# Kernel tuning notes

Measured on AMD Instinct MI355X. Metric: run time of the kernel, lower is better.

Reference implementation:

```python
import jax, jax.numpy as jnp
import numpy as np
import math

B, L, D, P = 2, 2048, 256, 32

def _lin_init(key, fan_in, shape):
    return jax.random.normal(key, shape, dtype=jnp.float32) / np.float32(math.sqrt(fan_in))

def setup_inputs() -> dict:
    key = jax.random.key(0)
    ks = jax.random.split(key, 16)
    return {
        "x": jax.random.normal(ks[0], (B, L, D), dtype=jnp.float32),
        "pos_phases": jax.random.normal(ks[1], (L, P), dtype=jnp.float32) * np.float32(math.pi),
        "w_pos_value": _lin_init(ks[2], D, (D, D)), "b_pos_value": jnp.zeros((D,), jnp.float32),
        "w_key": _lin_init(ks[3], D, (D, P)), "b_key": jnp.zeros((P,), jnp.float32),
        "w_kv": _lin_init(ks[4], D, (D, D)), "b_kv": jnp.zeros((D,), jnp.float32),
        "w_vg1": _lin_init(ks[5], 2 * D, (2 * D, D)), "b_vg1": jnp.zeros((D,), jnp.float32),
        "w_vg2": _lin_init(ks[6], D, (D, 1)), "b_vg2": jnp.zeros((1,), jnp.float32),
        "w_bg1": _lin_init(ks[7], D, (D, D // 2)), "b_bg1": jnp.zeros((D // 2,), jnp.float32),
        "w_bg2": _lin_init(ks[8], D // 2, (D // 2, 2)), "b_bg2": jnp.zeros((2,), jnp.float32),
        "ln_r_g": jnp.ones((D,), jnp.float32), "ln_r_b": jnp.zeros((D,), jnp.float32),
        "w_r1": _lin_init(ks[9], D, (D, 2 * D)), "b_r1": jnp.zeros((2 * D,), jnp.float32),
        "w_r2": _lin_init(ks[10], 2 * D, (2 * D, D)), "b_r2": jnp.zeros((D,), jnp.float32),
        "ln_o_g": jnp.ones((D,), jnp.float32), "ln_o_b": jnp.zeros((D,), jnp.float32),
        "w_out": _lin_init(ks[11], D, (D, D)), "b_out": jnp.zeros((D,), jnp.float32),
    }

def _ln(z, g, b, eps=1e-5):
    mu = z.mean(-1, keepdims=True)
    var = ((z - mu) ** 2).mean(-1, keepdims=True)
    return (z - mu) * jax.lax.rsqrt(var + eps) * g + b

def _shift1(z):
    # torch.roll(shifts=1, dims=1) then zero first position == shift right with zero pad
    return jnp.concatenate([jnp.zeros_like(z[:, :1]), z[:, :-1]], axis=1)

def reference(x, pos_phases, w_pos_value, b_pos_value, w_key, b_key, w_kv, b_kv,
              w_vg1, b_vg1, w_vg2, b_vg2, w_bg1, b_bg1, w_bg2, b_bg2,
              ln_r_g, ln_r_b, w_r1, b_r1, w_r2, b_r2, ln_o_g, ln_o_b, w_out, b_out):
    Bv, Lv, Dv = x.shape
    Pv = pos_phases.shape[1]
    inv_sqrt_p = np.float32(1.0 / math.sqrt(Pv))

    # --- positional memory ---
    pos_phasors = jnp.exp(1j * pos_phases)                      # (L,P) complex64
    pos_values = (x @ w_pos_value + b_pos_value).astype(jnp.complex64)  # (B,L,D)
    pos_bound = pos_phasors[None, :, :, None] * pos_values[:, :, None, :]  # (B,L,P,D)
    pos_memory = jnp.cumsum(pos_bound, axis=1)
    pos_query = jnp.exp(-1j * pos_phases)                       # (L,P)
    pos_retrieved = (pos_memory * pos_query[None, :, :, None]).sum(axis=2).real * inv_sqrt_p

    # --- content-based KV memory ---
    key_phases = jnp.tanh(x @ w_key + b_key) * np.float32(math.pi)  # (B,L,P)
    key_phasors = jnp.exp(1j * key_phases)
    kv_values = (x @ w_kv + b_kv).astype(jnp.complex64)         # (B,L,D)

    x_shifted = _shift1(x)
    gate_input = jnp.concatenate([x, x_shifted], axis=-1)       # (B,L,2D)
    h = jax.nn.gelu(gate_input @ w_vg1 + b_vg1, approximate=False)
    value_gates = jax.nn.sigmoid(h @ w_vg2 + b_vg2)             # (B,L,1)

    key_phasors_shifted = _shift1(key_phasors)                  # (B,L,P)
    kv_bound = (key_phasors_shifted[..., None] * kv_values[:, :, None, :]) \
               * value_gates[:, :, :, None].astype(jnp.complex64)  # (B,L,P,D)
    kv_memory = jnp.cumsum(kv_bound, axis=1)
    gate_cumsum = jnp.maximum(jnp.cumsum(value_gates, axis=1), 1.0)  # (B,L,1)
    kv_query = jnp.exp(-1j * key_phases)                        # (B,L,P)
    kv_retrieved = (kv_memory * kv_query[..., None]).sum(axis=2).real
    kv_retrieved = kv_retrieved / (jnp.sqrt(gate_cumsum) * np.float32(math.sqrt(Pv)))

    # --- blend, refine, output ---
    bg_h = jax.nn.gelu(x @ w_bg1 + b_bg1, approximate=False)
    blend = jax.nn.softmax(bg_h @ w_bg2 + b_bg2, axis=-1)       # (B,L,2)
    blended = blend[..., 0:1] * pos_retrieved + blend[..., 1:2] * kv_retrieved

    refined = jax.nn.gelu(_ln(blended, ln_r_g, ln_r_b) @ w_r1 + b_r1, approximate=False) @ w_r2 + b_r2
    return x + (_ln(refined, ln_o_g, ln_o_b) @ w_out + b_out)
```

## Files before the change

### kernel.cpp

```cpp
#include <hip/hip_runtime.h>
#include <math.h>

#define B_ 2
#define L_ 2048
#define D_ 256
#define P_ 32
#define NC_ 64
#define CL_ 32

#define INV_SQRT_P 0.17677669529663687f
#define PI_F 3.14159265358979323846f

typedef __attribute__((ext_vector_type(8))) short bf16x8;
typedef __attribute__((ext_vector_type(4))) float f32x4;

__device__ __forceinline__ float gelu_exact(float x){
    return 0.5f * x * (1.0f + erff(x * 0.70710678118654752f));
}

__device__ __forceinline__ unsigned short f2bf(float f){
    unsigned int u = __float_as_uint(f);
    u += 0x7FFFu + ((u >> 16) & 1u);
    return (unsigned short)(u >> 16);
}

__global__ __launch_bounds__(256) void k_prep(
    const float* __restrict__ pos_phases,
    const float* __restrict__ w_pv, const float* __restrict__ w_kv,
    const float* __restrict__ w_vg1, const float* __restrict__ w_bg1,
    const float* __restrict__ w_r1, const float* __restrict__ w_r2,
    const float* __restrict__ w_out, const float* __restrict__ w_key,
    unsigned short* __restrict__ wq,
    float* __restrict__ cpos, float* __restrict__ spos)
{
    int id = blockIdx.x * 256 + threadIdx.x;
    if (id < 630784){
        const float* src; int N; int local;
        if (id < 65536)       { src = w_pv;  N = 256; local = id; }
        else if (id < 131072) { src = w_kv;  N = 256; local = id - 65536; }
        else if (id < 262144) { src = w_vg1; N = 256; local = id - 131072; }
        else if (id < 294912) { src = w_bg1; N = 128; local = id - 262144; }
        else if (id < 425984) { src = w_r1;  N = 512; local = id - 294912; }
        else if (id < 557056) { src = w_r2;  N = 256; local = id - 425984; }
        else if (id < 622592) { src = w_out; N = 256; local = id - 557056; }
        else                  { src = w_key; N = 32;  local = id - 622592; }
        int j = local & 7, lane = (local >> 3) & 63, tile = local >> 9;
        int NT = N >> 4;
        int nt = tile % NT, kt = tile / NT;
        int row = kt * 32 + ((lane >> 4) << 3) + j;
        int col = nt * 16 + (lane & 15);
        wq[id] = f2bf(src[(size_t)row * N + col]);
    } else {
        int idx = id - 630784;
        float s, c;
        sincosf(pos_phases[idx], &s, &c);
        cpos[idx] = c;
        spos[idx] = s;
    }
}

__global__ __launch_bounds__(512) void k_proj(
    const float* __restrict__ x,
    const unsigned short* __restrict__ wq,
    const float* __restrict__ b_pv, const float* __restrict__ b_kv,
    const float* __restrict__ b_vg1,
    const float* __restrict__ w_vg2, const float* __restrict__ b_vg2,
    const float* __restrict__ b_bg1,
    const float* __restrict__ w_bg2, const float* __restrict__ b_bg2,
    const float* __restrict__ b_key,
    float* __restrict__ pv, float* __restrict__ kvv,
    float* __restrict__ ck, float* __restrict__ sk,
    float* __restrict__ vg, float* __restrict__ blend0, float* __restrict__ blend1)
{
    __shared__ float hbuf[16][257];
    __shared__ float bhbuf[16][129];
    __shared__ float kph[16][33];
    __shared__ float red[16][17], red2[16][17], red3[16][17];

    const int i = threadIdx.x;
    const int lane = i & 63, w = i >> 6;
    const int b = blockIdx.x >> 7, lt = blockIdx.x & 127, l0 = lt * 16;
    const int g = lane >> 4, c = lane & 15;

    bf16x8 xa[8], xs[8];
    {
        int row  = l0 + (lane & 15);
        int rowp = row - 1;
        const float* xr = x + (size_t)(b * L_ + row) * D_ + ((lane >> 4) << 3);
        #pragma unroll
        for (int kt = 0; kt < 8; ++kt){
            float4 a0 = *(const float4*)(xr + kt * 32);
            float4 a1 = *(const float4*)(xr + kt * 32 + 4);
            bf16x8 v;
            v[0] = (short)f2bf(a0.x); v[1] = (short)f2bf(a0.y);
            v[2] = (short)f2bf(a0.z); v[3] = (short)f2bf(a0.w);
            v[4] = (short)f2bf(a1.x); v[5] = (short)f2bf(a1.y);
            v[6] = (short)f2bf(a1.z); v[7] = (short)f2bf(a1.w);
            xa[kt] = v;
        }
        if (rowp >= 0){
            const float* xp = x + (size_t)(b * L_ + rowp) * D_ + ((lane >> 4) << 3);
            #pragma unroll
            for (int kt = 0; kt < 8; ++kt){
                float4 a0 = *(const float4*)(xp + kt * 32);
                float4 a1 = *(const float4*)(xp + kt * 32 + 4);
                bf16x8 v;
                v[0] = (short)f2bf(a0.x); v[1] = (short)f2bf(a0.y);
                v[2] = (short)f2bf(a0.z); v[3] = (short)f2bf(a0.w);
                v[4] = (short)f2bf(a1.x); v[5] = (short)f2bf(a1.y);
                v[6] = (short)f2bf(a1.z); v[7] = (short)f2bf(a1.w);
                xs[kt] = v;
            }
        } else {
            #pragma unroll
            for (int kt = 0; kt < 8; ++kt){
                bf16x8 v;
                #pragma unroll
                for (int j = 0; j < 8; ++j) v[j] = 0;
                xs[kt] = v;
            }
        }
    }

    const unsigned short* wpv  = wq;
    const unsigned short* wkv  = wq + 65536;
    const unsigned short* wvg1 = wq + 131072;
    const unsigned short* wbg1 = wq + 262144;
    const unsigned short* wkey = wq + 622592;

    for (int jb = w; jb < 58; jb += 8){
        f32x4 acc = {0.f, 0.f, 0.f, 0.f};
        if (jb < 2){
            int nt = jb;
            #pragma unroll
            for (int kt = 0; kt < 8; ++kt){
                bf16x8 bf = *(const bf16x8*)(wkey + (kt * 2 + nt) * 512 + lane * 8);
                acc = __builtin_amdgcn_mfma_f32_16x16x32_bf16(xa[kt], bf, acc, 0, 0, 0);
            }
            float bb = b_key[nt * 16 + c];
            #pragma unroll
            for (int r = 0; r < 4; ++r)
                kph[4 * g + r][nt * 16 + c] = acc[r] + bb;
        } else if (jb < 18){
            int nt = jb - 2;
            #pragma unroll
            for (int kt = 0; kt < 8; ++kt){
                bf16x8 bf = *(const bf16x8*)(wpv + (kt * 16 + nt) * 512 + lane * 8);
                acc = __builtin_amdgcn_mfma_f32_16x16x32_bf16(xa[kt], bf, acc, 0, 0, 0);
            }
            float bb = b_pv[nt * 16 + c];
            #pragma unroll
            for (int r = 0; r < 4; ++r)
                pv[(size_t)(b * L_ + l0 + 4 * g + r) * D_ + nt * 16 + c] = acc[r] + bb;
        } else if (jb < 34){
            int nt = jb - 18;
            #pragma unroll
            for (int kt = 0; kt < 8; ++kt){
                bf16x8 bf = *(const bf16x8*)(wkv + (kt * 16 + nt) * 512 + lane * 8);
                acc = __builtin_amdgcn_mfma_f32_16x16x32_bf16(xa[kt], bf, acc, 0, 0, 0);
            }
            float bb = b_kv[nt * 16 + c];
            #pragma unroll
            for (int r = 0; r < 4; ++r)
                kvv[(size_t)(b * L_ + l0 + 4 * g + r) * D_ + nt * 16 + c] = acc[r] + bb;
        } else if (jb < 50){
            int nt = jb - 34;
            #pragma unroll
            for (int kt = 0; kt < 8; ++kt){
                bf16x8 bf = *(const bf16x8*)(wvg1 + (kt * 16 + nt) * 512 + lane * 8);
                acc = __builtin_amdgcn_mfma_f32_16x16x32_bf16(xa[kt], bf, acc, 0, 0, 0);
            }
            #pragma unroll
            for (int kt = 8; kt < 16; ++kt){
                bf16x8 bf = *(const bf16x8*)(wvg1 + (kt * 16 + nt) * 512 + lane * 8);
                acc = __builtin_amdgcn_mfma_f32_16x16x32_bf16(xs[kt - 8], bf, acc, 0, 0, 0);
            }
            float bb = b_vg1[nt * 16 + c];
            #pragma unroll
            for (int r = 0; r < 4; ++r)
                hbuf[4 * g + r][nt * 16 + c] = gelu_exact(acc[r] + bb);
        } else {
            int nt = jb - 50;
            #pragma unroll
            for (int kt = 0; kt < 8; ++kt){
                bf16x8 bf = *(const bf16x8*)(wbg1 + (kt * 8 + nt) * 512 + lane * 8);
                acc = __builtin_amdgcn_mfma_f32_16x16x32_bf16(xa[kt], bf, acc, 0, 0, 0);
            }
            float bb = b_bg1[nt * 16 + c];
            #pragma unroll
            for (int r = 0; r < 4; ++r)
                bhbuf[4 * g + r][nt * 16 + c] = gelu_exact(acc[r] + bb);
        }
    }
    __syncthreads();

    {
        int t = i >> 5, p = i & 31;
        float a = tanhf(kph[t][p]) * PI_F;
        float s, cc;
        sincosf(a, &s, &cc);
        ck[(size_t)(b * L_ + l0 + t) * P_ + p] = cc;
        sk[(size_t)(b * L_ + l0 + t) * P_ + p] = s;
    }

    if (i < 256){
        int t = i >> 4, c2 = i & 15;
        float s = 0.f;
        #pragma unroll
        for (int m = 0; m < 16; ++m){ int dd = c2 + 16 * m; s += hbuf[t][dd] * w_vg2[dd]; }
        red[t][c2] = s;
    } else {
        int ii = i - 256;
        int t = ii >> 4, c2 = ii & 15;
        float s0 = 0.f, s1 = 0.f;
        #pragma unroll
        for (int m = 0; m < 8; ++m){
            int jj = c2 + 16 * m;
            float v = bhbuf[t][jj];
            s0 += v * w_bg2[jj * 2 + 0];
            s1 += v * w_bg2[jj * 2 + 1];
        }
        red2[t][c2] = s0; red3[t][c2] = s1;
    }
    __syncthreads();
    if (i < 16){
        float s = 0.f;
        #pragma unroll
        for (int c2 = 0; c2 < 16; ++c2) s += red[i][c2];
        s += b_vg2[0];
        vg[b * L_ + l0 + i] = 1.0f / (1.0f + expf(-s));
    } else if (i < 32){
        int t = i - 16;
        float s0 = 0.f, s1 = 0.f;
        #pragma unroll
        for (int c2 = 0; c2 < 16; ++c2){ s0 += red2[t][c2]; s1 += red3[t][c2]; }
        s0 += b_bg2[0]; s1 += b_bg2[1];
        float mx = fmaxf(s0, s1);
        float e0 = expf(s0 - mx), e1 = expf(s1 - mx);
        float inv = 1.0f / (e0 + e1);
        blend0[b * L_ + l0 + t] = e0 * inv;
        blend1[b * L_ + l0 + t] = e1 * inv;
    }
}

__global__ __launch_bounds__(256) void k_scan1(
    const float* __restrict__ cpos, const float* __restrict__ spos,
    const float* __restrict__ ck, const float* __restrict__ sk,
    const float* __restrict__ pv, const float* __restrict__ kvv,
    const float* __restrict__ vg,
    float* __restrict__ posSr, float* __restrict__ posSi,
    float* __restrict__ kvSr, float* __restrict__ kvSi,
    float* __restrict__ rnorm)
{
    const int z = blockIdx.z;
    const int c = blockIdx.x, b = blockIdx.y;
    const int i = threadIdx.x;
    if (z == 8){
        if (c != 0) return;
        float loc[8];
        float run = 0.f;
        #pragma unroll
        for (int m = 0; m < 8; ++m){ run += vg[b * L_ + i * 8 + m]; loc[m] = run; }
        __shared__ float part[256];
        part[i] = run;
        __syncthreads();
        for (int off = 1; off < 256; off <<= 1){
            float t = (i >= off) ? part[i - off] : 0.0f;
            __syncthreads();
            part[i] += t;
            __syncthreads();
        }
        float excl = part[i] - run;
        #pragma unroll
        for (int m = 0; m < 8; ++m){
            float gc = fmaxf(excl + loc[m], 1.0f);
            rnorm[b * L_ + i * 8 + m] = rsqrtf(gc) * INV_SQRT_P;
        }
        return;
    }
    const int type = z >> 2, pg = z & 3;
    const int d = i;
    const int p0 = pg * 8;
    float Sr[8], Si[8];
    #pragma unroll
    for (int j = 0; j < 8; ++j){ Sr[j] = 0.f; Si[j] = 0.f; }

    if (type == 0){
        for (int l = 0; l < CL_; ++l){
            int row = c * CL_ + l;
            float v = pv[(size_t)(b * L_ + row) * D_ + d];
            float4 c0 = *(const float4*)(cpos + row * P_ + p0);
            float4 c1 = *(const float4*)(cpos + row * P_ + p0 + 4);
            float4 s0 = *(const float4*)(spos + row * P_ + p0);
            float4 s1 = *(const float4*)(spos + row * P_ + p0 + 4);
            Sr[0] = fmaf(c0.x, v, Sr[0]); Si[0] = fmaf(s0.x, v, Si[0]);
            Sr[1] = fmaf(c0.y, v, Sr[1]); Si[1] = fmaf(s0.y, v, Si[1]);
            Sr[2] = fmaf(c0.z, v, Sr[2]); Si[2] = fmaf(s0.z, v, Si[2]);
            Sr[3] = fmaf(c0.w, v, Sr[3]); Si[3] = fmaf(s0.w, v, Si[3]);
            Sr[4] = fmaf(c1.x, v, Sr[4]); Si[4] = fmaf(s1.x, v, Si[4]);
            Sr[5] = fmaf(c1.y, v, Sr[5]); Si[5] = fmaf(s1.y, v, Si[5]);
            Sr[6] = fmaf(c1.z, v, Sr[6]); Si[6] = fmaf(s1.z, v, Si[6]);
            Sr[7] = fmaf(c1.w, v, Sr[7]); Si[7] = fmaf(s1.w, v, Si[7]);
        }
        #pragma unroll
        for (int j = 0; j < 8; ++j){
            size_t o = (size_t)((b * NC_ + c) * P_ + p0 + j) * D_ + d;
            posSr[o] = Sr[j]; posSi[o] = Si[j];
        }
    } else {
        float pc[8], ps[8];
        int srow = c * CL_ - 1;
        if (srow >= 0){
            float4 c0 = *(const float4*)(ck + ((size_t)b * L_ + srow) * P_ + p0);
            float4 c1 = *(const float4*)(ck + ((size_t)b * L_ + srow) * P_ + p0 + 4);
            float4 s0 = *(const float4*)(sk + ((size_t)b * L_ + srow) * P_ + p0);
            float4 s1 = *(const float4*)(sk + ((size_t)b * L_ + srow) * P_ + p0 + 4);
            pc[0]=c0.x; pc[1]=c0.y; pc[2]=c0.z; pc[3]=c0.w;
            pc[4]=c1.x; pc[5]=c1.y; pc[6]=c1.z; pc[7]=c1.w;
            ps[0]=s0.x; ps[1]=s0.y; ps[2]=s0.z; ps[3]=s0.w;
            ps[4]=s1.x; ps[5]=s1.y; ps[6]=s1.z; ps[7]=s1.w;
        } else {
            #pragma unroll
            for (int j = 0; j < 8; ++j){ pc[j] = 0.f; ps[j] = 0.f; }
        }
        for (int l = 0; l < CL_; ++l){
            int row = c * CL_ + l;
            float vv = kvv[(size_t)(b * L_ + row) * D_ + d] * vg[b * L_ + row];
            float4 c0 = *(const float4*)(ck + ((size_t)b * L_ + row) * P_ + p0);
            float4 c1 = *(const float4*)(ck + ((size_t)b * L_ + row) * P_ + p0 + 4);
            float4 s0 = *(const float4*)(sk + ((size_t)b * L_ + row) * P_ + p0);
            float4 s1 = *(const float4*)(sk + ((size_t)b * L_ + row) * P_ + p0 + 4);
            #pragma unroll
            for (int j = 0; j < 8; ++j){
                Sr[j] = fmaf(pc[j], vv, Sr[j]);
                Si[j] = fmaf(ps[j], vv, Si[j]);
            }
            pc[0]=c0.x; pc[1]=c0.y; pc[2]=c0.z; pc[3]=c0.w;
            pc[4]=c1.x; pc[5]=c1.y; pc[6]=c1.z; pc[7]=c1.w;
            ps[0]=s0.x; ps[1]=s0.y; ps[2]=s0.z; ps[3]=s0.w;
            ps[4]=s1.x; ps[5]=s1.y; ps[6]=s1.z; ps[7]=s1.w;
        }
        #pragma unroll
        for (int j = 0; j < 8; ++j){
            size_t o = (size_t)((b * NC_ + c) * P_ + p0 + j) * D_ + d;
            kvSr[o] = Sr[j]; kvSi[o] = Si[j];
        }
    }
}

__global__ __launch_bounds__(256) void k_prefix(
    float* __restrict__ posSr, float* __restrict__ posSi,
    float* __restrict__ kvSr, float* __restrict__ kvSi)
{
    __shared__ float4 tot_s[64][4];
    const int colLocal = threadIdx.x >> 2, seg = threadIdx.x & 3;
    const int col = blockIdx.x * 64 + colLocal;
    const int a = col >> 12;
    const int rem = col & 4095;
    const int b = rem >> 11;
    const int pd = (rem & 2047) * 4;
    float* A = (a == 0) ? posSr : (a == 1) ? posSi : (a == 2) ? kvSr : kvSi;
    float* base = A + (size_t)b * NC_ * (P_ * D_) + pd;

    float4 t[16];
    #pragma unroll
    for (int k = 0; k < 16; ++k)
        t[k] = *(const float4*)(base + (size_t)(seg * 16 + k) * (P_ * D_));
    float4 tot = {0.f, 0.f, 0.f, 0.f};
    #pragma unroll
    for (int k = 0; k < 16; ++k){
        tot.x += t[k].x; tot.y += t[k].y; tot.z += t[k].z; tot.w += t[k].w;
    }
    tot_s[colLocal][seg] = tot;
    __syncthreads();
    float4 run = {0.f, 0.f, 0.f, 0.f};
    #pragma unroll
    for (int s = 0; s < 3; ++s){
        if (s < seg){
            float4 v = tot_s[colLocal][s];
            run.x += v.x; run.y += v.y; run.z += v.z; run.w += v.w;
        }
    }
    #pragma unroll
    for (int k = 0; k < 16; ++k){
        float4 cur = t[k];
        *(float4*)(base + (size_t)(seg * 16 + k) * (P_ * D_)) = run;
        run.x += cur.x; run.y += cur.y; run.z += cur.z; run.w += cur.w;
    }
}

__global__ __launch_bounds__(256) void k_retrieve(
    const float* __restrict__ cpos, const float* __restrict__ spos,
    const float* __restrict__ ck, const float* __restrict__ sk,
    const float* __restrict__ pv, const float* __restrict__ kvv,
    const float* __restrict__ vg, const float* __restrict__ rnorm,
    const float* __restrict__ posSr, const float* __restrict__ posSi,
    const float* __restrict__ kvSr, const float* __restrict__ kvSi,
    float* __restrict__ posret, float* __restrict__ kvret)
{
    const int z = blockIdx.z;
    const int c = blockIdx.x, b = blockIdx.y;
    const int type = z >> 2, dquad = z & 3;
    const int lane = threadIdx.x & 63, wv = threadIdx.x >> 6;
    const int pg = lane >> 4, dl = lane & 15;
    const int d = dquad * 64 + wv * 16 + dl;
    const int p0 = pg * 8;

    float Sr[8], Si[8];

    if (type == 0){
        #pragma unroll
        for (int j = 0; j < 8; ++j){
            size_t o = (size_t)((b * NC_ + c) * P_ + p0 + j) * D_ + d;
            Sr[j] = posSr[o]; Si[j] = posSi[o];
        }
        for (int l = 0; l < CL_; ++l){
            int row = c * CL_ + l;
            float v = pv[(size_t)(b * L_ + row) * D_ + d];
            float4 c0 = *(const float4*)(cpos + row * P_ + p0);
            float4 c1 = *(const float4*)(cpos + row * P_ + p0 + 4);
            float4 s0 = *(const float4*)(spos + row * P_ + p0);
            float4 s1 = *(const float4*)(spos + row * P_ + p0 + 4);
            float r0 = 0.f, r1 = 0.f, r2 = 0.f, r3 = 0.f;
            Sr[0] = fmaf(c0.x, v, Sr[0]); r0 = fmaf(c0.x, Sr[0], r0);
            Si[0] = fmaf(s0.x, v, Si[0]); r1 = fmaf(s0.x, Si[0], r1);
            Sr[1] = fmaf(c0.y, v, Sr[1]); r2 = fmaf(c0.y, Sr[1], r2);
            Si[1] = fmaf(s0.y, v, Si[1]); r3 = fmaf(s0.y, Si[1], r3);
            Sr[2] = fmaf(c0.z, v, Sr[2]); r0 = fmaf(c0.z, Sr[2], r0);
            Si[2] = fmaf(s0.z, v, Si[2]); r1 = fmaf(s0.z, Si[2], r1);
            Sr[3] = fmaf(c0.w, v, Sr[3]); r2 = fmaf(c0.w, Sr[3], r2);
            Si[3] = fmaf(s0.w, v, Si[3]); r3 = fmaf(s0.w, Si[3], r3);
            Sr[4] = fmaf(c1.x, v, Sr[4]); r0 = fmaf(c1.x, Sr[4], r0);
            Si[4] = fmaf(s1.x, v, Si[4]); r1 = fmaf(s1.x, Si[4], r1);
            Sr[5] = fmaf(c1.y, v, Sr[5]); r2 = fmaf(c1.y, Sr[5], r2);
            Si[5] = fmaf(s1.y, v, Si[5]); r3 = fmaf(s1.y, Si[5], r3);
            Sr[6] = fmaf(c1.z, v, Sr[6]); r0 = fmaf(c1.z, Sr[6], r0);
            Si[6] = fmaf(s1.z, v, Si[6]); r1 = fmaf(s1.z, Si[6], r1);
            Sr[7] = fmaf(c1.w, v, Sr[7]); r2 = fmaf(c1.w, Sr[7], r2);
            Si[7] = fmaf(s1.w, v, Si[7]); r3 = fmaf(s1.w, Si[7], r3);
            float r = (r0 + r1) + (r2 + r3);
            r += __shfl_xor(r, 16, 64);
            r += __shfl_xor(r, 32, 64);
            if (pg == 0)
                posret[(size_t)(b * L_ + row) * D_ + d] = r * INV_SQRT_P;
        }
    } else {
        #pragma unroll
        for (int j = 0; j < 8; ++j){
            size_t o = (size_t)((b * NC_ + c) * P_ + p0 + j) * D_ + d;
            Sr[j] = kvSr[o]; Si[j] = kvSi[o];
        }
        float pc[8], ps[8];
        int srow = c * CL_ - 1;
        if (srow >= 0){
            float4 c0 = *(const float4*)(ck + ((size_t)b * L_ + srow) * P_ + p0);
            float4 c1 = *(const float4*)(ck + ((size_t)b * L_ + srow) * P_ + p0 + 4);
            float4 s0 = *(const float4*)(sk + ((size_t)b * L_ + srow) * P_ + p0);
            float4 s1 = *(const float4*)(sk + ((size_t)b * L_ + srow) * P_ + p0 + 4);
            pc[0]=c0.x; pc[1]=c0.y; pc[2]=c0.z; pc[3]=c0.w;
            pc[4]=c1.x; pc[5]=c1.y; pc[6]=c1.z; pc[7]=c1.w;
            ps[0]=s0.x; ps[1]=s0.y; ps[2]=s0.z; ps[3]=s0.w;
            ps[4]=s1.x; ps[5]=s1.y; ps[6]=s1.z; ps[7]=s1.w;
        } else {
            #pragma unroll
            for (int j = 0; j < 8; ++j){ pc[j] = 0.f; ps[j] = 0.f; }
        }
        for (int l = 0; l < CL_; ++l){
            int row = c * CL_ + l;
            float vv = kvv[(size_t)(b * L_ + row) * D_ + d] * vg[b * L_ + row];
            float rn = rnorm[b * L_ + row];
            float4 c0 = *(const float4*)(ck + ((size_t)b * L_ + row) * P_ + p0);
            float4 c1 = *(const float4*)(ck + ((size_t)b * L_ + row) * P_ + p0 + 4);
            float4 s0 = *(const float4*)(sk + ((size_t)b * L_ + row) * P_ + p0);
            float4 s1 = *(const float4*)(sk + ((size_t)b * L_ + row) * P_ + p0 + 4);
            float qc[8], qs[8];
            qc[0]=c0.x; qc[1]=c0.y; qc[2]=c0.z; qc[3]=c0.w;
            qc[4]=c1.x; qc[5]=c1.y; qc[6]=c1.z; qc[7]=c1.w;
            qs[0]=s0.x; qs[1]=s0.y; qs[2]=s0.z; qs[3]=s0.w;
            qs[4]=s1.x; qs[5]=s1.y; qs[6]=s1.z; qs[7]=s1.w;
            float r0 = 0.f, r1 = 0.f, r2 = 0.f, r3 = 0.f;
            #pragma unroll
            for (int j = 0; j < 8; ++j){
                Sr[j] = fmaf(pc[j], vv, Sr[j]);
                Si[j] = fmaf(ps[j], vv, Si[j]);
                if (j & 1){ r2 = fmaf(qc[j], Sr[j], r2); r3 = fmaf(qs[j], Si[j], r3); }
                else      { r0 = fmaf(qc[j], Sr[j], r0); r1 = fmaf(qs[j], Si[j], r1); }
                pc[j] = qc[j]; ps[j] = qs[j];
            }
            float r = (r0 + r1) + (r2 + r3);
            r += __shfl_xor(r, 16, 64);
            r += __shfl_xor(r, 32, 64);
            if (pg == 0)
                kvret[(size_t)(b * L_ + row) * D_ + d] = r * rn;
        }
    }
}

__global__ __launch_bounds__(512) void k_final(
    const float* __restrict__ x,
    const float* __restrict__ posret, const float* __restrict__ kvret,
    const float* __restrict__ blend0, const float* __restrict__ blend1,
    const unsigned short* __restrict__ wq,
    const float* __restrict__ ln_r_g, const float* __restrict__ ln_r_b,
    const float* __restrict__ b_r1, const float* __restrict__ b_r2,
    const float* __restrict__ ln_o_g, const float* __restrict__ ln_o_b,
    const float* __restrict__ b_out,
    float* __restrict__ out)
{
    __shared__ float zbuf[16][257];
    __shared__ __align__(16) unsigned short aA[8][512];
    __shared__ __align__(16) unsigned short aH[16][512];
    __shared__ float red[16][17], red2[16][17];
    __shared__ float mu[16], rs[16];

    const int i = threadIdx.x, lane = i & 63, w = i >> 6;
    const int b = blockIdx.x >> 7, l0 = (blockIdx.x & 127) * 16;
    const int g = lane >> 4, c = lane & 15;
    const unsigned short* wr1  = wq + 294912;
    const unsigned short* wr2  = wq + 425984;
    const unsigned short* wout = wq + 557056;

    {
        int t = i >> 5, c0 = (i & 31) * 8;
        size_t base = (size_t)(b * L_ + l0 + t) * D_ + c0;
        float w0 = blend0[b * L_ + l0 + t], w1 = blend1[b * L_ + l0 + t];
        #pragma unroll
        for (int m = 0; m < 8; ++m)
            zbuf[t][c0 + m] = w0 * posret[base + m] + w1 * kvret[base + m];
    }
    __syncthreads();

    if (i < 256){
        int t = i >> 4, c2 = i & 15;
        float s = 0.f, s2 = 0.f;
        #pragma unroll
        for (int m = 0; m < 16; ++m){ float v = zbuf[t][c2 + 16 * m]; s += v; s2 += v * v; }
        red[t][c2] = s; red2[t][c2] = s2;
    }
    __syncthreads();
    if (i < 16){
        float s = 0.f, s2 = 0.f;
        #pragma unroll
        for (int c2 = 0; c2 < 16; ++c2){ s += red[i][c2]; s2 += red2[i][c2]; }
        float mean = s * (1.0f / 256.0f);
        float var  = s2 * (1.0f / 256.0f) - mean * mean;
        mu[i] = mean; rs[i] = rsqrtf(var + 1e-5f);
    }
    __syncthreads();

    {
        int kt = i >> 6;
        int t2 = lane & 15, kb = kt * 32 + ((lane >> 4) << 3);
        float m_ = mu[t2], r_ = rs[t2];
        bf16x8 v8;
        #pragma unroll
        for (int j = 0; j < 8; ++j){
            int k = kb + j;
            float v = (zbuf[t2][k] - m_) * r_ * ln_r_g[k] + ln_r_b[k];
            v8[j] = (short)f2bf(v);
        }
        *(bf16x8*)&aA[kt][lane * 8] = v8;
    }
    __syncthreads();

    {
        bf16x8 afr[8];
        #pragma unroll
        for (int kt = 0; kt < 8; ++kt) afr[kt] = *(const bf16x8*)&aA[kt][lane * 8];
        for (int q = 0; q < 4; ++q){
            int nt = w + 8 * q;
            f32x4 acc = {0.f, 0.f, 0.f, 0.f};
            #pragma unroll
            for (int kt = 0; kt < 8; ++kt){
                bf16x8 bf = *(const bf16x8*)(wr1 + (kt * 32 + nt) * 512 + lane * 8);
                acc = __builtin_amdgcn_mfma_f32_16x16x32_bf16(afr[kt], bf, acc, 0, 0, 0);
            }
            float bb = b_r1[nt * 16 + c];
            #pragma unroll
            for (int r = 0; r < 4; ++r){
                float hv = gelu_exact(acc[r] + bb);
                int t = 4 * g + r, hcol = nt * 16 + c;
// ... 63 lines not shown
        #pragma unroll
        for (int kt = 0; kt < 8; ++kt) azr[kt] = *(const bf16x8*)&aA[kt][lane * 8];
        for (int q = 0; q < 2; ++q){
            int nt = w + 8 * q;
            f32x4 acc = {0.f, 0.f, 0.f, 0.f};
            #pragma unroll
            for (int kt = 0; kt < 8; ++kt){
                bf16x8 bf = *(const bf16x8*)(wout + (kt * 16 + nt) * 512 + lane * 8);
                acc = __builtin_amdgcn_mfma_f32_16x16x32_bf16(azr[kt], bf, acc, 0, 0, 0);
            }
            float bb = b_out[nt * 16 + c];
            #pragma unroll
            for (int r = 0; r < 4; ++r){
                size_t o = (size_t)(b * L_ + l0 + 4 * g + r) * D_ + nt * 16 + c;
                out[o] = x[o] + acc[r] + bb;
            }
        }
    }
}

extern "C" void kernel_launch(void* const* d_in, const int* in_sizes, int n_in,
                              void* d_out, int out_size, void* d_ws, size_t ws_size,
                              hipStream_t stream) {
    const float* x          = (const float*)d_in[0];
    const float* pos_phases = (const float*)d_in[1];
    const float* w_pv       = (const float*)d_in[2];
    const float* b_pv       = (const float*)d_in[3];
    const float* w_key      = (const float*)d_in[4];
    const float* b_key      = (const float*)d_in[5];
    const float* w_kv       = (const float*)d_in[6];
    const float* b_kv       = (const float*)d_in[7];
    const float* w_vg1      = (const float*)d_in[8];
    const float* b_vg1      = (const float*)d_in[9];
    const float* w_vg2      = (const float*)d_in[10];
    const float* b_vg2      = (const float*)d_in[11];
    const float* w_bg1      = (const float*)d_in[12];
    const float* b_bg1      = (const float*)d_in[13];
    const float* w_bg2      = (const float*)d_in[14];
    const float* b_bg2      = (const float*)d_in[15];
    const float* ln_r_g     = (const float*)d_in[16];
    const float* ln_r_b     = (const float*)d_in[17];
    const float* w_r1       = (const float*)d_in[18];
    const float* b_r1       = (const float*)d_in[19];
    const float* w_r2       = (const float*)d_in[20];
    const float* b_r2       = (const float*)d_in[21];
    const float* ln_o_g     = (const float*)d_in[22];
    const float* ln_o_b     = (const float*)d_in[23];
    const float* w_out      = (const float*)d_in[24];
    const float* b_out      = (const float*)d_in[25];
    float* out = (float*)d_out;

    float* ws = (float*)d_ws;
    size_t off = 0;
    float* cpos   = ws + off; off += (size_t)L_ * P_;
    float* spos   = ws + off; off += (size_t)L_ * P_;
    float* pv     = ws + off; off += (size_t)B_ * L_ * D_;
    float* kvv    = ws + off; off += (size_t)B_ * L_ * D_;
    float* ck     = ws + off; off += (size_t)B_ * L_ * P_;
    float* sk     = ws + off; off += (size_t)B_ * L_ * P_;
    float* vg     = ws + off; off += (size_t)B_ * L_;
    float* rnorm  = ws + off; off += (size_t)B_ * L_;
    float* blend0 = ws + off; off += (size_t)B_ * L_;
    float* blend1 = ws + off; off += (size_t)B_ * L_;
    float* posret = ws + off; off += (size_t)B_ * L_ * D_;
    float* kvret  = ws + off; off += (size_t)B_ * L_ * D_;
    float* posSr  = ws + off; off += (size_t)B_ * NC_ * P_ * D_;
    float* posSi  = ws + off; off += (size_t)B_ * NC_ * P_ * D_;
    float* kvSr   = ws + off; off += (size_t)B_ * NC_ * P_ * D_;
    float* kvSi   = ws + off; off += (size_t)B_ * NC_ * P_ * D_;
    unsigned short* wq = (unsigned short*)(ws + off); off += 630784 / 2;

    k_prep<<<2720, 256, 0, stream>>>(pos_phases,
        w_pv, w_kv, w_vg1, w_bg1, w_r1, w_r2, w_out, w_key,
        wq, cpos, spos);

    k_proj<<<B_ * 128, 512, 0, stream>>>(x, wq,
        b_pv, b_kv, b_vg1, w_vg2, b_vg2, b_bg1, w_bg2, b_bg2, b_key,
        pv, kvv, ck, sk, vg, blend0, blend1);

    k_scan1<<<dim3(NC_, B_, 9), 256, 0, stream>>>(cpos, spos, ck, sk, pv, kvv, vg,
                                                  posSr, posSi, kvSr, kvSi, rnorm);

    k_prefix<<<256, 256, 0, stream>>>(posSr, posSi, kvSr, kvSi);

    k_retrieve<<<dim3(NC_, B_, 8), 256, 0, stream>>>(cpos, spos, ck, sk, pv, kvv,
                                                     vg, rnorm,
                                                     posSr, posSi, kvSr, kvSi,
                                                     posret, kvret);

    k_final<<<B_ * 128, 512, 0, stream>>>(x, posret, kvret, blend0, blend1, wq,
        ln_r_g, ln_r_b, b_r1, b_r2, ln_o_g, ln_o_b, b_out, out);
}
```

Before: 89.07 us.

## Replace chunked complex scan with causal-masked MFMA attention formulation

Measured after the change: 148.5 us. +66.7%, slower.

```diff
diff --git a/kernel.cpp b/kernel.cpp
--- a/kernel.cpp
+++ b/kernel.cpp
@@ -5,14 +5,13 @@
 #define L_ 2048
 #define D_ 256
 #define P_ 32
-#define NC_ 64
-#define CL_ 32
 
 #define INV_SQRT_P 0.17677669529663687f
 #define PI_F 3.14159265358979323846f
 
 typedef __attribute__((ext_vector_type(8))) short bf16x8;
 typedef __attribute__((ext_vector_type(4))) float f32x4;
+typedef __attribute__((ext_vector_type(4))) unsigned short u16x4;
 
 __device__ __forceinline__ float gelu_exact(float x){
     return 0.5f * x * (1.0f + erff(x * 0.70710678118654752f));
@@ -31,7 +30,7 @@
     const float* __restrict__ w_r1, const float* __restrict__ w_r2,
     const float* __restrict__ w_out, const float* __restrict__ w_key,
     unsigned short* __restrict__ wq,
-    float* __restrict__ cpos, float* __restrict__ spos)
+    unsigned short* __restrict__ phib_pos)
 {
     int id = blockIdx.x * 256 + threadIdx.x;
     if (id < 630784){
@@ -52,10 +51,11 @@
         wq[id] = f2bf(src[(size_t)row * N + col]);
     } else {
         int idx = id - 630784;
+        int l = idx >> 5, p = idx & 31;
         float s, c;
         sincosf(pos_phases[idx], &s, &c);
-        cpos[idx] = c;
-        spos[idx] = s;
+        phib_pos[(size_t)l * 64 + p]      = f2bf(c);
+        phib_pos[(size_t)l * 64 + 32 + p] = f2bf(s);
     }
 }
 
@@ -68,14 +68,16 @@
     const float* __restrict__ b_bg1,
     const float* __restrict__ w_bg2, const float* __restrict__ b_bg2,
     const float* __restrict__ b_key,
-    float* __restrict__ pv, float* __restrict__ kvv,
-    float* __restrict__ ck, float* __restrict__ sk,
+    unsigned short* __restrict__ pvT, unsigned short* __restrict__ kvvT,
+    unsigned short* __restrict__ phib_kv,
     float* __restrict__ vg, float* __restrict__ blend0, float* __restrict__ blend1)
 {
     __shared__ float hbuf[16][257];
+    __shared__ float kvbuf[16][257];
     __shared__ float bhbuf[16][129];
     __shared__ float kph[16][33];
     __shared__ float red[16][17], red2[16][17], red3[16][17];
+    __shared__ float vgs[16];
 
     const int i = threadIdx.x;
     const int lane = i & 63, w = i >> 6;
@@ -149,9 +151,11 @@
                 acc = __builtin_amdgcn_mfma_f32_16x16x32_bf16(xa[kt], bf, acc, 0, 0, 0);
             }
             float bb = b_pv[nt * 16 + c];
-            #pragma unroll
-            for (int r = 0; r < 4; ++r)
-                pv[(size_t)(b * L_ + l0 + 4 * g + r) * D_ + nt * 16 + c] = acc[r] + bb;
+            int d = nt * 16 + c;
+            u16x4 pk;
+            pk[0] = f2bf(acc[0] + bb); pk[1] = f2bf(acc[1] + bb);
+            pk[2] = f2bf(acc[2] + bb); pk[3] = f2bf(acc[3] + bb);
+            *(u16x4*)(pvT + (size_t)(b * 256 + d) * 2048 + l0 + 4 * g) = pk;
         } else if (jb < 34){
             int nt = jb - 18;
             #pragma unroll
@@ -162,7 +166,7 @@
             float bb = b_kv[nt * 16 + c];
             #pragma unroll
             for (int r = 0; r < 4; ++r)
-                kvv[(size_t)(b * L_ + l0 + 4 * g + r) * D_ + nt * 16 + c] = acc[r] + bb;
+                kvbuf[4 * g + r][nt * 16 + c] = acc[r] + bb;
         } else if (jb < 50){
             int nt = jb - 34;
             #pragma unroll
@@ -199,8 +203,9 @@
         float a = tanhf(kph[t][p]) * PI_F;
         float s, cc;
         sincosf(a, &s, &cc);
-        ck[(size_t)(b * L_ + l0 + t) * P_ + p] = cc;
-        sk[(size_t)(b * L_ + l0 + t) * P_ + p] = s;
+        size_t rowo = (size_t)(b * L_ + l0 + t) * 64;
+        phib_kv[rowo + p]      = f2bf(cc);
+        phib_kv[rowo + 32 + p] = f2bf(s);
     }
 
     if (i < 256){
@@ -228,7 +233,9 @@
         #pragma unroll
         for (int c2 = 0; c2 < 16; ++c2) s += red[i][c2];
         s += b_vg2[0];
-        vg[b * L_ + l0 + i] = 1.0f / (1.0f + expf(-s));
+        float gv = 1.0f / (1.0f + expf(-s));
+        vg[b * L_ + l0 + i] = gv;
+        vgs[i] = gv;
     } else if (i < 32){
         int t = i - 16;
         float s0 = 0.f, s1 = 0.f;
@@ -241,265 +248,171 @@
         blend0[b * L_ + l0 + t] = e0 * inv;
         blend1[b * L_ + l0 + t] = e1 * inv;
     }
-}
-
-__global__ __launch_bounds__(256) void k_scan1(
-    const float* __restrict__ cpos, const float* __restrict__ spos,
-    const float* __restrict__ ck, const float* __restrict__ sk,
-    const float* __restrict__ pv, const float* __restrict__ kvv,
-    const float* __restrict__ vg,
-    float* __restrict__ posSr, float* __restrict__ posSi,
-    float* __restrict__ kvSr, float* __restrict__ kvSi,
-    float* __restrict__ rnorm)
+    __syncthreads();
+
+    {
+        int d = i & 255, tg = i >> 8;
+        bf16x8 pk;
+        #pragma unroll
+        for (int m = 0; m < 8; ++m){
+            int tok = tg * 8 + m;
+            pk[m] = (short)f2bf(kvbuf[tok][d] * vgs[tok]);
+        }
+        *(bf16x8*)(kvvT + (size_t)(b * 256 + d) * 2048 + l0 + tg * 8) = pk;
+    }
+}
+
+__global__ __launch_bounds__(256) void k_gatecum(const float* __restrict__ vg,
+                                                 float* __restrict__ rnorm){
+    int b = blockIdx.x, i = threadIdx.x;
+    float loc[8];
+    float run = 0.f;
+    #pragma unroll
+    for (int m = 0; m < 8; ++m){ run += vg[b * L_ + i * 8 + m]; loc[m] = run; }
+    __shared__ float part[256];
+    part[i] = run;
+    __syncthreads();
+    for (int off = 1; off < 256; off <<= 1){
+        float t = (i >= off) ? part[i - off] : 0.0f;
+        __syncthreads();
+        part[i] += t;
+        __syncthreads();
+    }
+    float excl = part[i] - run;
+    #pragma unroll
+    for (int m = 0; m < 8; ++m){
+        float gc = fmaxf(excl + loc[m], 1.0f);
+        rnorm[b * L_ + i * 8 + m] = rsqrtf(gc) * INV_SQRT_P;
+    }
+}
+
+__global__ __launch_bounds__(256) void k_flash(
+    const unsigned short* __restrict__ phib_pos,
+    const unsigned short* __restrict__ phib_kv,
+    const unsigned short* __restrict__ pvT,
+    const unsigned short* __restrict__ kvvT,
+    const float* __restrict__ rnorm,
+    const float* __restrict__ blend0, const float* __restrict__ blend1,
+    float* __restrict__ blended)
 {
-    const int z = blockIdx.z;
-    const int c = blockIdx.x, b = blockIdx.y;
-    const int i = threadIdx.x;
-    if (z == 8){
-        if (c != 0) return;
-        float loc[8];
-        float run = 0.f;
-        #pragma unroll
-        for (int m = 0; m < 8; ++m){ run += vg[b * L_ + i * 8 + m]; loc[m] = run; }
-        __shared__ float part[256];
-        part[i] = run;
-        __syncthreads();
-        for (int off = 1; off < 256; off <<= 1){
-            float t = (i >= off) ? part[i - off] : 0.0f;
-            __syncthreads();
-            part[i] += t;
-            __syncthreads();
-        }
-        float excl = part[i] - run;
-        #pragma unroll
-        for (int m = 0; m < 8; ++m){
-            float gc = fmaxf(excl + loc[m], 1.0f);
-            rnorm[b * L_ + i * 8 + m] = rsqrtf(gc) * INV_SQRT_P;
-        }
-        return;
-    }
-    const int type = z >> 2, pg = z & 3;
-    const int d = i;
-    const int p0 = pg * 8;
-    float Sr[8], Si[8];
+    __shared__ float redb[4][16][132];
+    __shared__ __align__(16) unsigned short scrP[4][16][40];
+    __shared__ __align__(16) unsigned short scrK[4][16][40];
+
+    const int qt = 127 - (blockIdx.x & 127);
+    const int dhalf = blockIdx.x >> 7;
+    const int b = blockIdx.y;
+    const int w = threadIdx.x >> 6, lane = threadIdx.x & 63;
+    const int g = lane >> 4, c = lane & 15;
+    const int q0 = qt * 16, d0 = dhalf * 128;
+
+    bf16x8 aqp[2], aqk[2];
+    {
+        const unsigned short* pp = phib_pos + (size_t)(q0 + c) * 64 + 8 * g;
+        aqp[0] = *(const bf16x8*)(pp);
+        aqp[1] = *(const bf16x8*)(pp + 32);
+        const unsigned short* pk = phib_kv + (size_t)(b * L_ + q0 + c) * 64 + 8 * g;
+        aqk[0] = *(const bf16x8*)(pk);
+        aqk[1] = *(const bf16x8*)(pk + 32);
+    }
+    f32x4 accP[8], accK[8];
     #pragma unroll
-    for (int j = 0; j < 8; ++j){ Sr[j] = 0.f; Si[j] = 0.f; }
-
-    if (type == 0){
-        for (int l = 0; l < CL_; ++l){
-            int row = c * CL_ + l;
-            float v = pv[(size_t)(b * L_ + row) * D_ + d];
-            float4 c0 = *(const float4*)(cpos + row * P_ + p0);
-            float4 c1 = *(const float4*)(cpos + row * P_ + p0 + 4);
-            float4 s0 = *(const float4*)(spos + row * P_ + p0);
-            float4 s1 = *(const float4*)(spos + row * P_ + p0 + 4);
-            Sr[0] = fmaf(c0.x, v, Sr[0]); Si[0] = fmaf(s0.x, v, Si[0]);
-            Sr[1] = fmaf(c0.y, v, Sr[1]); Si[1] = fmaf(s0.y, v, Si[1]);
-            Sr[2] = fmaf(c0.z, v, Sr[2]); Si[2] = fmaf(s0.z, v, Si[2]);
-            Sr[3] = fmaf(c0.w, v, Sr[3]); Si[3] = fmaf(s0.w, v, Si[3]);
-            Sr[4] = fmaf(c1.x, v, Sr[4]); Si[4] = fmaf(s1.x, v, Si[4]);
-            Sr[5] = fmaf(c1.y, v, Sr[5]); Si[5] = fmaf(s1.y, v, Si[5]);
-            Sr[6] = fmaf(c1.z, v, Sr[6]); Si[6] = fmaf(s1.z, v, Si[6]);
-            Sr[7] = fmaf(c1.w, v, Sr[7]); Si[7] = fmaf(s1.w, v, Si[7]);
-        }
-        #pragma unroll
-        for (int j = 0; j < 8; ++j){
-            size_t o = (size_t)((b * NC_ + c) * P_ + p0 + j) * D_ + d;
-            posSr[o] = Sr[j]; posSi[o] = Si[j];
-        }
-    } else {
-        float pc[8], ps[8];
-        int srow = c * CL_ - 1;
-        if (srow >= 0){
-            float4 c0 = *(const float4*)(ck + ((size_t)b * L_ + srow) * P_ + p0);
-            float4 c1 = *(const float4*)(ck + ((size_t)b * L_ + srow) * P_ + p0 + 4);
-            float4 s0 = *(const float4*)(sk + ((size_t)b * L_ + srow) * P_ + p0);
-            float4 s1 = *(const float4*)(sk + ((size_t)b * L_ + srow) * P_ + p0 + 4);
-            pc[0]=c0.x; pc[1]=c0.y; pc[2]=c0.z; pc[3]=c0.w;
-            pc[4]=c1.x; pc[5]=c1.y; pc[6]=c1.z; pc[7]=c1.w;
-            ps[0]=s0.x; ps[1]=s0.y; ps[2]=s0.z; ps[3]=s0.w;
-            ps[4]=s1.x; ps[5]=s1.y; ps[6]=s1.z; ps[7]=s1.w;
-        } else {
-            #pragma unroll
-            for (int j = 0; j < 8; ++j){ pc[j] = 0.f; ps[j] = 0.f; }
-        }
-        for (int l = 0; l < CL_; ++l){
-            int row = c * CL_ + l;
-            float vv = kvv[(size_t)(b * L_ + row) * D_ + d] * vg[b * L_ + row];
-            float4 c0 = *(const float4*)(ck + ((size_t)b * L_ + row) * P_ + p0);
-            float4 c1 = *(const float4*)(ck + ((size_t)b * L_ + row) * P_ + p0 + 4);
-            float4 s0 = *(const float4*)(sk + ((size_t)b * L_ + row) * P_ + p0);
-            float4 s1 = *(const float4*)(sk + ((size_t)b * L_ + row) * P_ + p0 + 4);
-            #pragma unroll
-            for (int j = 0; j < 8; ++j){
-                Sr[j] = fmaf(pc[j], vv, Sr[j]);
-                Si[j] = fmaf(ps[j], vv, Si[j]);
-            }
-            pc[0]=c0.x; pc[1]=c0.y; pc[2]=c0.z; pc[3]=c0.w;
-            pc[4]=c1.x; pc[5]=c1.y; pc[6]=c1.z; pc[7]=c1.w;
-            ps[0]=s0.x; ps[1]=s0.y; ps[2]=s0.z; ps[3]=s0.w;
-            ps[4]=s1.x; ps[5]=s1.y; ps[6]=s1.z; ps[7]=s1.w;
-        }
-        #pragma unroll
-        for (int j = 0; j < 8; ++j){
-            size_t o = (size_t)((b * NC_ + c) * P_ + p0 + j) * D_ + d;
-            kvSr[o] = Sr[j]; kvSi[o] = Si[j];
-        }
-    }
-}
-
-__global__ __launch_bounds__(256) void k_prefix(
-    float* __restrict__ posSr, float* __restrict__ posSi,
-    float* __restrict__ kvSr, float* __restrict__ kvSi)
-{
-    __shared__ float4 tot_s[64][4];
-    const int colLocal = threadIdx.x >> 2, seg = threadIdx.x & 3;
-    const int col = blockIdx.x * 64 + colLocal;
-    const int a = col >> 12;
-    const int rem = col & 4095;
-    const int b = rem >> 11;
-    const int pd = (rem & 2047) * 4;
-    float* A = (a == 0) ? posSr : (a == 1) ? posSi : (a == 2) ? kvSr : kvSi;
-    float* base = A + (size_t)b * NC_ * (P_ * D_) + pd;
-
-    float4 t[16];
+    for (int dt = 0; dt < 8; ++dt){
+        accP[dt] = (f32x4){0.f, 0.f, 0.f, 0.f};
+        accK[dt] = (f32x4){0.f, 0.f, 0.f, 0.f};
+    }
+
+    const int nsteps = ((qt + 1) * 16 + 31) >> 5;
+    for (int m = w; m < nsteps; m += 4){
+        const int k0 = m * 32;
+        f32x4 sP[2], sK[2];
+        #pragma unroll
+        for (int nt = 0; nt < 2; ++nt){
+            sP[nt] = (f32x4){0.f, 0.f, 0.f, 0.f};
+            sK[nt] = (f32x4){0.f, 0.f, 0.f, 0.f};
+            int key = k0 + nt * 16 + c;
+            const unsigned short* bp = phib_pos + (size_t)key * 64 + 8 * g;
+            bf16x8 bf0 = *(const bf16x8*)(bp);
+            bf16x8 bf1 = *(const bf16x8*)(bp + 32);
+            sP[nt] = __builtin_amdgcn_mfma_f32_16x16x32_bf16(aqp[0], bf0, sP[nt], 0, 0, 0);
+            sP[nt] = __builtin_amdgcn_mfma_f32_16x16x32_bf16(aqp[1], bf1, sP[nt], 0, 0, 0);
+            int srow = key - 1;
+            bf16x8 bk0, bk1;
+            if (srow >= 0){
+                const unsigned short* bk = phib_kv + (size_t)(b * L_ + srow) * 64 + 8 * g;
+                bk0 = *(const bf16x8*)(bk);
+                bk1 = *(const bf16x8*)(bk + 32);
+            } else {
+                #pragma unroll
+                for (int j = 0; j < 8; ++j){ bk0[j] = 0; bk1[j] = 0; }
+            }
+            sK[nt] = __builtin_amdgcn_mfma_f32_16x16x32_bf16(aqk[0], bk0, sK[nt], 0, 0, 0);
+            sK[nt] = __builtin_amdgcn_mfma_f32_16x16x32_bf16(aqk[1], bk1, sK[nt], 0, 0, 0);
+        }
+        #pragma unroll
+        for (int nt = 0; nt < 2; ++nt){
+            int kk = nt * 16 + c;
+            #pragma unroll
+            for (int r = 0; r < 4; ++r){
+                bool keep = (k0 + kk) <= (q0 + 4 * g + r);
+                scrP[w][4 * g + r][kk] = keep ? f2bf(sP[nt][r]) : (unsigned short)0;
+                scrK[w][4 * g + r][kk] = keep ? f2bf(sK[nt][r]) : (unsigned short)0;
+            }
+        }
+        bf16x8 ap = *(const bf16x8*)&scrP[w][c][8 * g];
+        bf16x8 ak = *(const bf16x8*)&scrK[w][c][8 * g];
+        const unsigned short* vp = pvT  + (size_t)(b * 256 + d0 + c) * 2048 + k0 + 8 * g;
+        const unsigned short* vk = kvvT + (size_t)(b * 256 + d0 + c) * 2048 + k0 + 8 * g;
+        #pragma unroll
+        for (int dt = 0; dt < 8; ++dt){
+            bf16x8 bv = *(const bf16x8*)(vp + (size_t)dt * 16 * 2048);
+            accP[dt] = __builtin_amdgcn_mfma_f32_16x16x32_bf16(ap, bv, accP[dt], 0, 0, 0);
+            bf16x8 bgv = *(const bf16x8*)(vk + (size_t)dt * 16 * 2048);
+            accK[dt] = __builtin_amdgcn_mfma_f32_16x16x32_bf16(ak, bgv, accK[dt], 0, 0, 0);
+        }
+    }
+
     #pragma unroll
-    for (int k = 0; k < 16; ++k)
-        t[k] = *(const float4*)(base + (size_t)(seg * 16 + k) * (P_ * D_));
-    float4 tot = {0.f, 0.f, 0.f, 0.f};
+    for (int dt = 0; dt < 8; ++dt)
+        #pragma unroll
+        for (int r = 0; r < 4; ++r)
+            redb[w][4 * g + r][dt * 16 + c] = accP[dt][r];
+    __syncthreads();
+    float psum[8];
+    {
+        int t = threadIdx.x;
+        #pragma unroll
+        for (int i2 = 0; i2 < 8; ++i2){
+            int e = i2 * 256 + t;
+            int q = e >> 7, dl = e & 127;
+            psum[i2] = redb[0][q][dl] + redb[1][q][dl] + redb[2][q][dl] + redb[3][q][dl];
+        }
+    }
+    __syncthreads();
     #pragma unroll
-    for (int k = 0; k < 16; ++k){
-        tot.x += t[k].x; tot.y += t[k].y; tot.z += t[k].z; tot.w += t[k].w;
-    }
-    tot_s[colLocal][seg] = tot;
-    __syncthreads();
-    float4 run = {0.f, 0.f, 0.f, 0.f};
-    #pragma unroll
-    for (int s = 0; s < 3; ++s){
-        if (s < seg){
-            float4 v = tot_s[colLocal][s];
-            run.x += v.x; run.y += v.y; run.z += v.z; run.w += v.w;
-        }
-    }
-    #pragma unroll
-    for (int k = 0; k < 16; ++k){
-        float4 cur = t[k];
-        *(float4*)(base + (size_t)(seg * 16 + k) * (P_ * D_)) = run;
-        run.x += cur.x; run.y += cur.y; run.z += cur.z; run.w += cur.w;
-    }
-}
-
-__global__ __launch_bounds__(256) void k_retrieve(
-    const float* __restrict__ cpos, const float* __restrict__ spos,
-    const float* __restrict__ ck, const float* __restrict__ sk,
-    const float* __restrict__ pv, const float* __restrict__ kvv,
-    const float* __restrict__ vg, const float* __restrict__ rnorm,
-    const float* __restrict__ posSr, const float* __restrict__ posSi,
-    const float* __restrict__ kvSr, const float* __restrict__ kvSi,
-    float* __restrict__ posret, float* __restrict__ kvret)
-{
-    const int z = blockIdx.z;
-    const int c = blockIdx.x, b = blockIdx.y;
-    const int type = z >> 2, dquad = z & 3;
-    const int lane = threadIdx.x & 63, wv = threadIdx.x >> 6;
-    const int pg = lane >> 4, dl = lane & 15;
-    const int d = dquad * 64 + wv * 16 + dl;
-    const int p0 = pg * 8;
-
-    float Sr[8], Si[8];
-
-    if (type == 0){
-        #pragma unroll
-        for (int j = 0; j < 8; ++j){
-            size_t o = (size_t)((b * NC_ + c) * P_ + p0 + j) * D_ + d;
-            Sr[j] = posSr[o]; Si[j] = posSi[o];
-        }
-        for (int l = 0; l < CL_; ++l){
-            int row = c * CL_ + l;
-            float v = pv[(size_t)(b * L_ + row) * D_ + d];
-            float4 c0 = *(const float4*)(cpos + row * P_ + p0);
-            float4 c1 = *(const float4*)(cpos + row * P_ + p0 + 4);
-            float4 s0 = *(const float4*)(spos + row * P_ + p0);
-            float4 s1 = *(const float4*)(spos + row * P_ + p0 + 4);
-            float r0 = 0.f, r1 = 0.f, r2 = 0.f, r3 = 0.f;
-            Sr[0] = fmaf(c0.x, v, Sr[0]); r0 = fmaf(c0.x, Sr[0], r0);
-            Si[0] = fmaf(s0.x, v, Si[0]); r1 = fmaf(s0.x, Si[0], r1);
-            Sr[1] = fmaf(c0.y, v, Sr[1]); r2 = fmaf(c0.y, Sr[1], r2);
-            Si[1] = fmaf(s0.y, v, Si[1]); r3 = fmaf(s0.y, Si[1], r3);
-            Sr[2] = fmaf(c0.z, v, Sr[2]); r0 = fmaf(c0.z, Sr[2], r0);
-            Si[2] = fmaf(s0.z, v, Si[2]); r1 = fmaf(s0.z, Si[2], r1);
-            Sr[3] = fmaf(c0.w, v, Sr[3]); r2 = fmaf(c0.w, Sr[3], r2);
-            Si[3] = fmaf(s0.w, v, Si[3]); r3 = fmaf(s0.w, Si[3], r3);
-            Sr[4] = fmaf(c1.x, v, Sr[4]); r0 = fmaf(c1.x, Sr[4], r0);
-            Si[4] = fmaf(s1.x, v, Si[4]); r1 = fmaf(s1.x, Si[4], r1);
-            Sr[5] = fmaf(c1.y, v, Sr[5]); r2 = fmaf(c1.y, Sr[5], r2);
-            Si[5] = fmaf(s1.y, v, Si[5]); r3 = fmaf(s1.y, Si[5], r3);
-            Sr[6] = fmaf(c1.z, v, Sr[6]); r0 = fmaf(c1.z, Sr[6], r0);
-            Si[6] = fmaf(s1.z, v, Si[6]); r1 = fmaf(s1.z, Si[6], r1);
-            Sr[7] = fmaf(c1.w, v, Sr[7]); r2 = fmaf(c1.w, Sr[7], r2);
-            Si[7] = fmaf(s1.w, v, Si[7]); r3 = fmaf(s1.w, Si[7], r3);
-            float r = (r0 + r1) + (r2 + r3);
-            r += __shfl_xor(r, 16, 64);
-            r += __shfl_xor(r, 32, 64);
-            if (pg == 0)
-                posret[(size_t)(b * L_ + row) * D_ + d] = r * INV_SQRT_P;
-        }
-    } else {
-        #pragma unroll
-        for (int j = 0; j < 8; ++j){
-            size_t o = (size_t)((b * NC_ + c) * P_ + p0 + j) * D_ + d;
-            Sr[j] = kvSr[o]; Si[j] = kvSi[o];
-        }
-        float pc[8], ps[8];
-        int srow = c * CL_ - 1;
-        if (srow >= 0){
-            float4 c0 = *(const float4*)(ck + ((size_t)b * L_ + srow) * P_ + p0);
-            float4 c1 = *(const float4*)(ck + ((size_t)b * L_ + srow) * P_ + p0 + 4);
-            float4 s0 = *(const float4*)(sk + ((size_t)b * L_ + srow) * P_ + p0);
-            float4 s1 = *(const float4*)(sk + ((size_t)b * L_ + srow) * P_ + p0 + 4);
-            pc[0]=c0.x; pc[1]=c0.y; pc[2]=c0.z; pc[3]=c0.w;
-            pc[4]=c1.x; pc[5]=c1.y; pc[6]=c1.z; pc[7]=c1.w;
-            ps[0]=s0.x; ps[1]=s0.y; ps[2]=s0.z; ps[3]=s0.w;
-            ps[4]=s1.x; ps[5]=s1.y; ps[6]=s1.z; ps[7]=s1.w;
-        } else {
-            #pragma unroll
-            for (int j = 0; j < 8; ++j){ pc[j] = 0.f; ps[j] = 0.f; }
-        }
-        for (int l = 0; l < CL_; ++l){
-            int row = c * CL_ + l;
-            float vv = kvv[(size_t)(b * L_ + row) * D_ + d] * vg[b * L_ + row];
-            float rn = rnorm[b * L_ + row];
-            float4 c0 = *(const float4*)(ck + ((size_t)b * L_ + row) * P_ + p0);
-            float4 c1 = *(const float4*)(ck + ((size_t)b * L_ + row) * P_ + p0 + 4);
-            float4 s0 = *(const float4*)(sk + ((size_t)b * L_ + row) * P_ + p0);
-            float4 s1 = *(const float4*)(sk + ((size_t)b * L_ + row) * P_ + p0 + 4);
-            float qc[8], qs[8];
-            qc[0]=c0.x; qc[1]=c0.y; qc[2]=c0.z; qc[3]=c0.w;
-            qc[4]=c1.x; qc[5]=c1.y; qc[6]=c1.z; qc[7]=c1.w;
-            qs[0]=s0.x; qs[1]=s0.y; qs[2]=s0.z; qs[3]=s0.w;
-            qs[4]=s1.x; qs[5]=s1.y; qs[6]=s1.z; qs[7]=s1.w;
-            float r0 = 0.f, r1 = 0.f, r2 = 0.f, r3 = 0.f;
-            #pragma unroll
-            for (int j = 0; j < 8; ++j){
-                Sr[j] = fmaf(pc[j], vv, Sr[j]);
-                Si[j] = fmaf(ps[j], vv, Si[j]);
-                if (j & 1){ r2 = fmaf(qc[j], Sr[j], r2); r3 = fmaf(qs[j], Si[j], r3); }
-                else      { r0 = fmaf(qc[j], Sr[j], r0); r1 = fmaf(qs[j], Si[j], r1); }
-                pc[j] = qc[j]; ps[j] = qs[j];
-            }
-            float r = (r0 + r1) + (r2 + r3);
-            r += __shfl_xor(r, 16, 64);
-            r += __shfl_xor(r, 32, 64);
-            if (pg == 0)
-                kvret[(size_t)(b * L_ + row) * D_ + d] = r * rn;
+    for (int dt = 0; dt < 8; ++dt)
+        #pragma unroll
+        for (int r = 0; r < 4; ++r)
+            redb[w][4 * g + r][dt * 16 + c] = accK[dt][r];
+    __syncthreads();
+    {
+        int t = threadIdx.x;
+        #pragma unroll
+        for (int i2 = 0; i2 < 8; ++i2){
+            int e = i2 * 256 + t;
+            int q = e >> 7, dl = e & 127;
+            float ks = redb[0][q][dl] + redb[1][q][dl] + redb[2][q][dl] + redb[3][q][dl];
+            int ql = b * L_ + q0 + q;
+            float val = blend0[ql] * INV_SQRT_P * psum[i2]
+                      + blend1[ql] * rnorm[ql] * ks;
+            blended[(size_t)ql * D_ + d0 + dl] = val;
         }
     }
 }
 
 __global__ __launch_bounds__(512) void k_final(
     const float* __restrict__ x,
-    const float* __restrict__ posret, const float* __restrict__ kvret,
-    const float* __restrict__ blend0, const float* __restrict__ blend1,
+    const float* __restrict__ blended,
     const unsigned short* __restrict__ wq,
     const float* __restrict__ ln_r_g, const float* __restrict__ ln_r_b,
     const float* __restrict__ b_r1, const float* __restrict__ b_r2,
@@ -522,11 +435,9 @@
 
     {
         int t = i >> 5, c0 = (i & 31) * 8;
-        size_t base = (size_t)(b * L_ + l0 + t) * D_ + c0;
-        float w0 = blend0[b * L_ + l0 + t], w1 = blend1[b * L_ + l0 + t];
-        #pragma unroll
-        for (int m = 0; m < 8; ++m)
-            zbuf[t][c0 + m] = w0 * posret[base + m] + w1 * kvret[base + m];
+        const float* src = blended + (size_t)(b * L_ + l0 + t) * D_ + c0;
+        #pragma unroll
+        for (int m = 0; m < 8; ++m) zbuf[t][c0 + m] = src[m];
     }
     __syncthreads();
 
@@ -696,42 +607,30 @@
 
     float* ws = (float*)d_ws;
     size_t off = 0;
-    float* cpos   = ws + off; off += (size_t)L_ * P_;
-    float* spos   = ws + off; off += (size_t)L_ * P_;
-    float* pv     = ws + off; off += (size_t)B_ * L_ * D_;
-    float* kvv    = ws + off; off += (size_t)B_ * L_ * D_;
-    float* ck     = ws + off; off += (size_t)B_ * L_ * P_;
-    float* sk     = ws + off; off += (size_t)B_ * L_ * P_;
     float* vg     = ws + off; off += (size_t)B_ * L_;
     float* rnorm  = ws + off; off += (size_t)B_ * L_;
     float* blend0 = ws + off; off += (size_t)B_ * L_;
     float* blend1 = ws + off; off += (size_t)B_ * L_;
-    float* posret = ws + off; off += (size_t)B_ * L_ * D_;
-    float* kvret  = ws + off; off += (size_t)B_ * L_ * D_;
-    float* posSr  = ws + off; off += (size_t)B_ * NC_ * P_ * D_;
-    float* posSi  = ws + off; off += (size_t)B_ * NC_ * P_ * D_;
-    float* kvSr   = ws + off; off += (size_t)B_ * NC_ * P_ * D_;
-    float* kvSi   = ws + off; off += (size_t)B_ * NC_ * P_ * D_;
-    unsigned short* wq = (unsigned short*)(ws + off); off += 630784 / 2;
+    float* blended= ws + off; off += (size_t)B_ * L_ * D_;
+    unsigned short* wq       = (unsigned short*)(ws + off); off += 630784 / 2;
+    unsigned short* phib_pos = (unsigned short*)(ws + off); off += (size_t)L_ * 64 / 2;
+    unsigned short* phib_kv  = (unsigned short*)(ws + off); off += (size_t)B_ * L_ * 64 / 2;
+    unsigned short* pvT      = (unsigned short*)(ws + off); off += (size_t)B_ * 256 * 2048 / 2;
+    unsigned short* kvvT     = (unsigned short*)(ws + off); off += (size_t)B_ * 256 * 2048 / 2;
 
     k_prep<<<2720, 256, 0, stream>>>(pos_phases,
         w_pv, w_kv, w_vg1, w_bg1, w_r1, w_r2, w_out, w_key,
-        wq, cpos, spos);
+        wq, phib_pos);
 
     k_proj<<<B_ * 128, 512, 0, stream>>>(x, wq,
         b_pv, b_kv, b_vg1, w_vg2, b_vg2, b_bg1, w_bg2, b_bg2, b_key,
-        pv, kvv, ck, sk, vg, blend0, blend1);
-
-    k_scan1<<<dim3(NC_, B_, 9), 256, 0, stream>>>(cpos, spos, ck, sk, pv, kvv, vg,
-                                                  posSr, posSi, kvSr, kvSi, rnorm);
-
-    k_prefix<<<256, 256, 0, stream>>>(posSr, posSi, kvSr, kvSi);
-
-    k_retrieve<<<dim3(NC_, B_, 8), 256, 0, stream>>>(cpos, spos, ck, sk, pv, kvv,
-                                                     vg, rnorm,
-                                                     posSr, posSi, kvSr, kvSi,
-                                                     posret, kvret);
-
-    k_final<<<B_ * 128, 512, 0, stream>>>(x, posret, kvret, blend0, blend1, wq,
+        pvT, kvvT, phib_kv, vg, blend0, blend1);
+
+    k_gatecum<<<B_, 256, 0, stream>>>(vg, rnorm);
+
+    k_flash<<<dim3(256, B_), 256, 0, stream>>>(phib_pos, phib_kv, pvT, kvvT,
+                                               rnorm, blend0, blend1, blended);
+
+    k_final<<<B_ * 128, 512, 0, stream>>>(x, blended, wq,
         ln_r_g, ln_r_b, b_r1, b_r2, ln_o_g, ln_o_b, b_out, out);
 }
```
